# Kernel tuning notes

Measured on AMD Instinct MI355X. Metric: run time of the kernel, lower is better.

The kernel has to match this reference:

```python
import jax, jax.numpy as jnp
import numpy as np
from jax import lax

BETA_CONTENT = 1.0   # content_addressing default beta
BETA_TOPK = 10.0     # top_k_attention default beta
GAMMA = 1.5          # location sharpening
ERASE = 0.5          # erase_strength for write
EPS = 1e-8
NEG = -1.0e9

N_SLOTS, SLOT_D, BATCH, K = 65536, 256, 512, 64


def _l2norm(x):
    # F.normalize: x / max(||x||, 1e-12)
    n = jnp.sqrt(jnp.sum(x * x, axis=-1, keepdims=True))
    return x / jnp.maximum(n, 1e-12)


def setup_inputs() -> dict:
    key = jax.random.key(0)
    k1, k2, k3, k4, k5 = jax.random.split(key, 5)
    return {
        "memory": jax.random.normal(k1, (N_SLOTS, SLOT_D), dtype=jnp.float32) * 0.1,
        "query": jax.random.normal(k2, (BATCH, SLOT_D), dtype=jnp.float32),
        "value": jax.random.normal(k3, (BATCH, SLOT_D), dtype=jnp.float32),
        "prev_weights": jax.random.uniform(k4, (BATCH, N_SLOTS), dtype=jnp.float32),
        "shift_weights": jax.random.uniform(k5, (3,), dtype=jnp.float32),
        "k": K,
    }


def reference(memory, query, value, prev_weights, shift_weights, k):
    B, N = query.shape[0], memory.shape[0]
    # --- content addressing: cosine sim + softmax ---
    qn = _l2norm(query)                      # [B,D]
    mn = _l2norm(memory)                     # [N,D]
    sim = qn @ mn.T                          # [B,N]
    w_content = jax.nn.softmax(BETA_CONTENT * sim, axis=-1)
    read_content = w_content @ memory        # [B,D] read via content weights

    # --- top-k attention: soft threshold mask + softmax ---
    kk = min(int(k), N)
    topk_vals, _ = lax.top_k(sim, kk)        # [B,kk]
    thr = topk_vals[:, -1:]                  # kth largest similarity
    mask = jax.nn.sigmoid(BETA_TOPK * (sim - thr))
    w_topk = jax.nn.softmax(BETA_TOPK * sim + (1.0 - mask) * NEG, axis=-1)
    read_topk = w_topk @ memory              # [B,D]

    # --- location addressing: conv1d shift (padding=1) + gamma sharpen ---
    p = jnp.pad(prev_weights, ((0, 0), (1, 1)))  # [B,N+2]
    shifted = (p[:, :-2] * shift_weights[0]
               + p[:, 1:-1] * shift_weights[1]
               + p[:, 2:] * shift_weights[2])     # [B,N]
    sharp = shifted ** GAMMA
    w_loc = sharp / (jnp.sum(sharp, axis=-1, keepdims=True) + EPS)

    # --- write: softmax(address), multiplicative erase, additive write ---
    w_write = jax.nn.softmax(w_loc, axis=-1)          # write() softmaxes its input
    erase_factor = jnp.prod(1.0 - w_write * ERASE, axis=0)   # [N] sequential erases fused
    new_mem = memory * erase_factor[:, None] + w_write.T @ value  # [N,D]

    return jnp.concatenate([read_content.reshape(-1),
                            read_topk.reshape(-1),
                            new_mem.reshape(-1)])
```

## Files before the change

### kernel.cpp

```cpp
#include <hip/hip_runtime.h>
#include <math.h>

#define BATCH   512
#define NSLOTS  65536
#define DIM     256

#define RB      64
#define NROWG   (BATCH/RB)
#define NCG     64
#define CPG     (NSLOTS/NCG)
#define ST      32
#define NTILES  (CPG/ST)
#define DELTA   0.009f

#define WS_QN   0
#define WS_RN   (WS_QN + BATCH*DIM)
#define WS_WST  (WS_RN + NSLOTS)
#define WS_DEN  (WS_WST + BATCH*4)
#define WS_SST  (WS_DEN + BATCH)
#define WS_VT   (WS_SST + BATCH*NCG*16*4)
#define WS_MN   (WS_VT + (BATCH*DIM)/2)
#define WS_MT   (WS_MN + ((size_t)NSLOTS*DIM)/2)

typedef __attribute__((ext_vector_type(8))) short bf16x8;
typedef __attribute__((ext_vector_type(4))) float f32x4;

__device__ inline unsigned short f2b(float x){
  unsigned u = __float_as_uint(x);
  unsigned r = u + 0x7FFFu + ((u >> 16) & 1u);
  return (unsigned short)(r >> 16);
}
__device__ inline float b2f(unsigned short b){
  return __uint_as_float(((unsigned)b) << 16);
}

__device__ __forceinline__ void gl16(const void* g, void* l){
  __builtin_amdgcn_global_load_lds(
      (__attribute__((address_space(1))) void*)g,
      (__attribute__((address_space(3))) void*)l, 16, 0, 0);
}

#define SBAR_LGKM() do{ asm volatile("s_waitcnt lgkmcnt(0)" ::: "memory"); \
                        __builtin_amdgcn_s_barrier();                      \
                        asm volatile("" ::: "memory"); }while(0)
#define SBAR_ALL()  do{ asm volatile("s_waitcnt vmcnt(0) lgkmcnt(0)" ::: "memory"); \
                        __builtin_amdgcn_s_barrier();                               \
                        asm volatile("" ::: "memory"); }while(0)

__global__ __launch_bounds__(256) void k_qnorm(const float* __restrict__ q, float* __restrict__ qn){
  int b = blockIdx.x, t = threadIdx.x;
  float v = q[b*DIM + t];
  __shared__ float red[256];
  red[t] = v*v;
  __syncthreads();
  for (int s = 128; s > 0; s >>= 1){
    if (t < s) red[t] += red[t+s];
    __syncthreads();
  }
  float n = fmaxf(sqrtf(red[0]), 1e-12f);
  qn[b*DIM + t] = v / n;
}

__global__ __launch_bounds__(256) void k_mnprep(const float* __restrict__ mem,
                                                float* __restrict__ rn,
                                                unsigned short* __restrict__ MN){
  __shared__ float rns[64];
  int t = threadIdx.x;
  int s0 = blockIdx.x * 64;
  int w = t >> 6, ln = t & 63;
  #pragma unroll
  for (int it = 0; it < 16; ++it){
    int r = it*4 + w;
    float4 v = ((const float4*)(mem + (size_t)(s0 + r)*DIM))[ln];
    float s = v.x*v.x + v.y*v.y + v.z*v.z + v.w*v.w;
    #pragma unroll
    for (int off = 32; off > 0; off >>= 1) s += __shfl_xor(s, off, 64);
    if (ln == 0){
      float inv = 1.0f / fmaxf(sqrtf(s), 1e-12f);
      rns[r] = inv; rn[s0 + r] = inv;
    }
  }
  __syncthreads();
  #pragma unroll
  for (int j = 0; j < 8; ++j){
    int id = j*256 + t;
    int r = id >> 5;
    int c = id & 31;
    float inv = rns[r];
    const float4* p = (const float4*)(mem + (size_t)(s0 + r)*DIM + c*8);
    float4 a = p[0], b = p[1];
    bf16x8 o;
    o[0]=(short)f2b(a.x*inv); o[1]=(short)f2b(a.y*inv); o[2]=(short)f2b(a.z*inv); o[3]=(short)f2b(a.w*inv);
    o[4]=(short)f2b(b.x*inv); o[5]=(short)f2b(b.y*inv); o[6]=(short)f2b(b.z*inv); o[7]=(short)f2b(b.w*inv);
    *(bf16x8*)&MN[(size_t)(s0 + r)*DIM + ((c ^ (r & 7))*8)] = o;
  }
}

__global__ __launch_bounds__(256) void k_mtprep(const float* __restrict__ mem, unsigned short* __restrict__ MT){
  __shared__ __align__(16) unsigned short tile[64][68];
  int sb = (blockIdx.x >> 2)*64, dd = (blockIdx.x & 3)*64;
  int t = threadIdx.x;
  int w = t >> 6, ln = t & 63;
  #pragma unroll
  for (int k = 0; k < 4; ++k){
    int sl = w*16 + k*4 + (ln >> 4);
    int doff = (ln & 15)*4;
    float4 f = *(const float4*)&mem[(size_t)(sb + sl)*DIM + dd + doff];
    tile[doff+0][sl] = f2b(f.x);
    tile[doff+1][sl] = f2b(f.y);
    tile[doff+2][sl] = f2b(f.z);
    tile[doff+3][sl] = f2b(f.w);
  }
  __syncthreads();
  #pragma unroll
  for (int k = 0; k < 4; ++k){
    int dl = w*16 + k*4 + (ln >> 4);
    int boff = (ln & 15)*4;
    int B = boff >> 5;
    int p = (boff >> 3) & 3;
    int pp = p ^ ((dl >> 1) & 3);
    int off = B*32 + pp*8 + (boff & 7);
    *(short4*)&MT[(size_t)(dd + dl)*NSLOTS + sb + off] = *(const short4*)&tile[dl][boff];
  }
}

__global__ __launch_bounds__(256) void k_prep(const float* __restrict__ val, unsigned short* __restrict__ VT){
  __shared__ __align__(16) unsigned short tile[64][68];
  int bb = (blockIdx.x >> 2)*64, dd = (blockIdx.x & 3)*64;
  int t = threadIdx.x;
  int w = t >> 6, ln = t & 63;
  #pragma unroll
  for (int k = 0; k < 4; ++k){
    int bl = w*16 + k*4 + (ln >> 4);
    int doff = (ln & 15)*4;
    float4 f = *(const float4*)&val[(size_t)(bb + bl)*DIM + dd + doff];
    tile[doff+0][bl] = f2b(f.x);
    tile[doff+1][bl] = f2b(f.y);
    tile[doff+2][bl] = f2b(f.z);
    tile[doff+3][bl] = f2b(f.w);
  }
  __syncthreads();
  #pragma unroll
  for (int k = 0; k < 4; ++k){
    int dl = w*16 + k*4 + (ln >> 4);
    int boff = (ln & 15)*4;
    int c  = (bb + boff) >> 5;
    int p  = (boff >> 3) & 3;
    int pp = p ^ ((dl >> 1) & 3);
    size_t addr = (size_t)c*8192 + (size_t)(dd + dl)*32 + pp*8 + (boff & 7);
    *(short4*)&VT[addr] = *(const short4*)&tile[dl][boff];
  }
}

__global__ __launch_bounds__(256) void k_wstats(const float* __restrict__ prev, const float* __restrict__ sw,
                                                float* __restrict__ wst){
  int b = blockIdx.x, t = threadIdx.x;
  float s0 = sw[0], s1 = sw[1], s2 = sw[2];
  const float* p = prev + (size_t)b*NSLOTS;
  const float4* p4 = (const float4*)p;
  __shared__ float rs[256];
  float lsum = 0.f;
  for (int i4 = t; i4 < NSLOTS/4; i4 += 256){
    float4 f = p4[i4];
    float lft = (i4 > 0) ? p[4*i4 - 1] : 0.f;
    float rgt = (i4 < NSLOTS/4 - 1) ? p[4*i4 + 4] : 0.f;
    float sh0 = s0*lft + s1*f.x + s2*f.y;
    float sh1 = s0*f.x + s1*f.y + s2*f.z;
    float sh2 = s0*f.y + s1*f.z + s2*f.w;
    float sh3 = s0*f.z + s1*f.w + s2*rgt;
    lsum += sh0*sqrtf(sh0) + sh1*sqrtf(sh1) + sh2*sqrtf(sh2) + sh3*sqrtf(sh3);
  }
  rs[t] = lsum;
  __syncthreads();
  for (int s = 128; s > 0; s >>= 1){
    if (t < s) rs[t] += rs[t+s];
    __syncthreads();
  }
  float inv_d = 1.0f / (rs[0] + 1e-8f);
  __syncthreads();
  float lz = 0.f;
  for (int i4 = t; i4 < NSLOTS/4; i4 += 256){
    float4 f = p4[i4];
    float lft = (i4 > 0) ? p[4*i4 - 1] : 0.f;
    float rgt = (i4 < NSLOTS/4 - 1) ? p[4*i4 + 4] : 0.f;
    float sh0 = s0*lft + s1*f.x + s2*f.y;
    float sh1 = s0*f.x + s1*f.y + s2*f.z;
    float sh2 = s0*f.y + s1*f.z + s2*f.w;
    float sh3 = s0*f.z + s1*f.w + s2*rgt;
    lz += __expf(sh0*sqrtf(sh0)*inv_d) + __expf(sh1*sqrtf(sh1)*inv_d)
        + __expf(sh2*sqrtf(sh2)*inv_d) + __expf(sh3*sqrtf(sh3)*inv_d);
  }
  rs[t] = lz;
  __syncthreads();
  for (int s = 128; s > 0; s >>= 1){
    if (t < s) rs[t] += rs[t+s];
    __syncthreads();
  }
  if (t == 0){
    float4 o; o.x = inv_d; o.y = 1.0f/rs[0]; o.z = 0.f; o.w = 0.f;
    ((float4*)wst)[b] = o;
  }
}

__global__ __launch_bounds__(256) void k_wft(const float* __restrict__ prev, const float* __restrict__ sw,
                                             const float* __restrict__ wst, unsigned short* __restrict__ WFT){
  __shared__ __align__(16) unsigned short T[64][72];
  int bs = ((int)blockIdx.x & 7) * 64;
  int ss = ((int)blockIdx.x >> 3) * 64;
  int t = threadIdx.x;
  float s0 = sw[0], s1 = sw[1], s2 = sw[2];
  int rr = t >> 4;
  int cc = t & 15;
  #pragma unroll
  for (int pass = 0; pass < 4; ++pass){
    int bl = pass*16 + rr;
    int b = bs + bl;
    const float* p = prev + (size_t)b*NSLOTS + ss;
    float2 st = *(const float2*)&wst[b*4];
    int s = cc*4;
    float4 f = *(const float4*)(p + s);
    int gs = ss + s;
    float lft = (gs > 0) ? p[s-1] : 0.f;
    float rgt = (gs + 4 < NSLOTS) ? p[s+4] : 0.f;
    float sh0 = s0*lft + s1*f.x + s2*f.y;
    float sh1 = s0*f.x + s1*f.y + s2*f.z;
    float sh2 = s0*f.y + s1*f.z + s2*f.w;
    float sh3 = s0*f.z + s1*f.w + s2*rgt;
    T[s+0][bl] = f2b(__expf(sh0*sqrtf(sh0)*st.x)*st.y);
    T[s+1][bl] = f2b(__expf(sh1*sqrtf(sh1)*st.x)*st.y);
    T[s+2][bl] = f2b(__expf(sh2*sqrtf(sh2)*st.x)*st.y);
    T[s+3][bl] = f2b(__expf(sh3*sqrtf(sh3)*st.x)*st.y);
  }
  __syncthreads();
  int sr = t >> 3;
  int ch = t & 7;
  #pragma unroll
  for (int k = 0; k < 2; ++k){
    int row = k*32 + sr;
    int c  = (bs >> 5) + (ch >> 2);
    int pp = (ch & 3) ^ ((row >> 1) & 3);
    size_t addr = (size_t)(ss >> 6)*32768 + (size_t)c*2048 + (size_t)row*32 + pp*8;
    *(bf16x8*)&WFT[addr] = *(const bf16x8*)&T[row][ch*8];
  }
}

__global__ __launch_bounds__(256, 2) void k_simfused(
    const float* __restrict__ qn,
    const unsigned short* __restrict__ MN,
    const unsigned short* __restrict__ MT,
    float* __restrict__ outc, float* __restrict__ denom, float* __restrict__ sst)
{
  __shared__ __align__(16) unsigned short Ms[2][32*256];
  __shared__ __align__(16) unsigned short Md[2][256*32];
  __shared__ __align__(16) unsigned short Plds[64*40];

  int cg = blockIdx.x, rg = blockIdx.y;
  int t = threadIdx.x;
  int w = t >> 6;
  int lane = t & 63;
  int l = lane & 15;
  int q = lane >> 4;
  int row0 = rg * RB;

  bf16x8 qa[8];
  {
    int qrow = row0 + 16*w + l;
    #pragma unroll
    for (int kk = 0; kk < 8; ++kk){
      const float4* qp = (const float4*)&qn[(size_t)qrow*DIM + 32*kk + 8*q];
      float4 a0 = qp[0], a1 = qp[1];
      bf16x8 v;
      v[0]=(short)f2b(a0.x); v[1]=(short)f2b(a0.y); v[2]=(short)f2b(a0.z); v[3]=(short)f2b(a0.w);
      v[4]=(short)f2b(a1.x); v[5]=(short)f2b(a1.y); v[6]=(short)f2b(a1.z); v[7]=(short)f2b(a1.w);
      qa[kk] = v;
    }
  }

  const char* msP = (const char*)MN + (size_t)cg*CPG*512 + (size_t)w*4096 + (size_t)lane*16;
  const char* mtP = (const char*)MT + (size_t)(w*64 + (lane>>2))*((size_t)NSLOTS*2)
                                    + (size_t)cg*CPG*2 + (size_t)(lane&3)*16;

  auto STAGE = [&](int tl, int buf){
    size_t mso = (size_t)tl*16384;
    size_t mto = (size_t)tl*64;
    #pragma unroll
    for (int j = 0; j < 4; ++j)
      gl16(msP + mso + (size_t)j*1024, &Ms[buf][w*2048 + j*512]);
    #pragma unroll
    for (int j = 0; j < 4; ++j)
      gl16(mtP + mto + (size_t)j*2097152, &Md[buf][w*2048 + j*512]);
  };

  f32x4 accO[16];
  #pragma unroll
  for (int c = 0; c < 16; ++c) accO[c] = (f32x4){0.f,0.f,0.f,0.f};

  float dsum[4] = {0.f,0.f,0.f,0.f};
  float tv0[4] = {-1e30f,-1e30f,-1e30f,-1e30f}, tv1[4] = {-1e30f,-1e30f,-1e30f,-1e30f};
  int   ti0[4] = {0,0,0,0}, ti1[4] = {0,0,0,0};

  STAGE(0, 0);
  SBAR_ALL();

  int r7 = l & 7;
  int sw2 = (q ^ ((l >> 1) & 3)) * 8;

  for (int tile = 0; tile < NTILES; ++tile){
    int cur = tile & 1;
    if (tile + 1 < NTILES) STAGE(tile + 1, cur ^ 1);
    int i0 = cg*CPG + tile*ST;

    const unsigned short* msb = &Ms[cur][0];
    f32x4 S0 = (f32x4){0.f,0.f,0.f,0.f}, S1 = (f32x4){0.f,0.f,0.f,0.f};
    #pragma unroll
    for (int kk = 0; kk < 8; ++kk){
      int c0 = ((4*kk + q) ^ r7) * 8;
      bf16x8 b0 = *(const bf16x8*)&msb[(l     )*256 + c0];
      bf16x8 b1 = *(const bf16x8*)&msb[(16 + l)*256 + c0];
      S0 = __builtin_amdgcn_mfma_f32_16x16x32_bf16(qa[kk], b0, S0, 0, 0, 0);
      S1 = __builtin_amdgcn_mfma_f32_16x16x32_bf16(qa[kk], b1, S1, 0, 0, 0);
    }

    #pragma unroll
    for (int c = 0; c < 2; ++c){
      int slot = i0 + 16*c + l;
      #pragma unroll
      for (int reg = 0; reg < 4; ++reg){
        float v = (c == 0) ? S0[reg] : S1[reg];
        bool g0 = v > tv0[reg];
        bool g1 = v > tv1[reg];
        float ov0 = tv0[reg]; int oi0 = ti0[reg];
        tv1[reg] = g0 ? ov0 : (g1 ? v : tv1[reg]);
        ti1[reg] = g0 ? oi0 : (g1 ? slot : ti1[reg]);
        tv0[reg] = g0 ? v : tv0[reg];
        ti0[reg] = g0 ? slot : ti0[reg];
        unsigned short wb = f2b(__expf(v));
        dsum[reg] += b2f(wb);
        Plds[(16*w + 4*q + reg)*40 + 16*c + l] = (short)wb;
      }
    }
    SBAR_LGKM();

    bf16x8 pa = *(const bf16x8*)&Plds[(16*w + l)*40 + 8*q];
    const unsigned short* mdb = &Md[cur][0];
    #pragma unroll
    for (int ct = 0; ct < 16; ++ct){
      bf16x8 b = *(const bf16x8*)&mdb[(16*ct + l)*32 + sw2];
      accO[ct] = __builtin_amdgcn_mfma_f32_16x16x32_bf16(pa, b, accO[ct], 0, 0, 0);
    }
    SBAR_ALL();
  }

  #pragma unroll
  for (int reg = 0; reg < 4; ++reg){
    float s = dsum[reg];
    s += __shfl_xor(s, 1, 64); s += __shfl_xor(s, 2, 64);
    s += __shfl_xor(s, 4, 64); s += __shfl_xor(s, 8, 64);
    if (l == 0) atomicAdd(&denom[row0 + 16*w + 4*q + reg], s);
  }
  #pragma unroll
  for (int reg = 0; reg < 4; ++reg){
    int row = row0 + 16*w + 4*q + reg;
    size_t base = (((size_t)row*NCG + cg)*16 + l)*2;
    float2* S2 = (float2*)sst;
    S2[base + 0] = make_float2(tv0[reg], __int_as_float(ti0[reg]));
    S2[base + 1] = make_float2(tv1[reg], __int_as_float(ti1[reg]));
  }
  #pragma unroll
  for (int ct = 0; ct < 16; ++ct){
    #pragma unroll
    for (int reg = 0; reg < 4; ++reg){
      int row = row0 + 16*w + 4*q + reg;
      atomicAdd(&outc[(size_t)row*DIM + 16*ct + l], accO[ct][reg]);
    }
  }
}

__global__ __launch_bounds__(256) void k_finish(const float* __restrict__ sst, const float* __restrict__ denom,
                                                const float* __restrict__ qn, const float* __restrict__ rn,
                                                const float* __restrict__ mem,
                                                float* __restrict__ outc, float* __restrict__ outk){
  int row = blockIdx.x, t = threadIdx.x;
  __shared__ float red[256];
  __shared__ int cnt;
  __shared__ int cidx[128];
  __shared__ float csim[128];
  __shared__ int bestIdx;
  const float2* S = (const float2*)sst + (size_t)row*NCG*16*2;
  float2 e[8];
  float lmax = -1e30f;
  #pragma unroll
  for (int k = 0; k < 8; ++k){ e[k] = S[t*8 + k]; lmax = fmaxf(lmax, e[k].x); }
  red[t] = lmax;
  __syncthreads();
  for (int s = 128; s > 0; s >>= 1){
    if (t < s) red[t] = fmaxf(red[t], red[t+s]);
    __syncthreads();
  }
  float M = red[0];
  if (t == 0) cnt = 0;
  __syncthreads();
  #pragma unroll
  for (int k = 0; k < 8; ++k){
    if (e[k].x >= M - DELTA){
      int p = atomicAdd(&cnt, 1);
      if (p < 128) cidx[p] = __float_as_int(e[k].y);
    }
  }
  __syncthreads();
  int n = min(cnt, 128);
  int wv = t >> 6, ln = t & 63;
  for (int ci = wv; ci < n; ci += 4){
    int slot = cidx[ci];
    float4 a = ((const float4*)&qn[(size_t)row*DIM])[ln];
    float4 b = ((const float4*)&mem[(size_t)slot*DIM])[ln];
    float s = a.x*b.x + a.y*b.y + a.z*b.z + a.w*b.w;
    #pragma unroll
    for (int off = 32; off > 0; off >>= 1) s += __shfl_xor(s, off, 64);
    if (ln == 0) csim[ci] = s * rn[slot];
  }
  __syncthreads();
  if (t == 0){
    float bv = -1e30f; int bi = 0x7fffffff;
    for (int i = 0; i < n; ++i){
      float v = csim[i]; int id = cidx[i];
      if (v > bv || (v == bv && id < bi)){ bv = v; bi = id; }
    }
    bestIdx = bi;
  }
  __syncthreads();
  float inv = 1.0f / denom[row];
  outc[(size_t)row*DIM + t] *= inv;
  outk[(size_t)row*DIM + t] = mem[(size_t)bestIdx*DIM + t];
}

__global__ __launch_bounds__(256, 4) void k_newmem(const float* __restrict__ mem,
                                                const unsigned short* __restrict__ VT2,
                                                const unsigned short* __restrict__ WFT2,
                                                float* __restrict__ outm){
  __shared__ __align__(16) unsigned short VB[2][256*32];
  __shared__ __align__(16) unsigned short WB[2][64*32];

  int t = threadIdx.x;
  int i0 = blockIdx.x * 64;
  int w = t >> 6;
  int lane = t & 63;
  int l = lane & 15, q = lane >> 4;

  const char* vbase = (const char*)VT2 + (size_t)w*4096 + (size_t)lane*16;
  const char* wbase = (const char*)WFT2 + (size_t)blockIdx.x*65536 + (size_t)w*1024 + (size_t)lane*16;

  auto STAGE = [&](int c, int buf){
    #pragma unroll
    for (int j = 0; j < 4; ++j)
      gl16(vbase + (size_t)c*16384 + (size_t)j*1024, &VB[buf][w*2048 + j*512]);
    gl16(wbase + (size_t)c*4096, &WB[buf][w*512]);
  };

  f32x4 accO[16];
  #pragma unroll
  for (int c = 0; c < 16; ++c) accO[c] = (f32x4){0.f,0.f,0.f,0.f};
  float epl = 1.0f;

  STAGE(0, 0);
  SBAR_ALL();

  int sw2 = (q ^ ((l >> 1) & 3)) * 8;

  #pragma unroll 1
  for (int c = 0; c < 16; ++c){
    int cur = c & 1;
    if (c + 1 < 16) STAGE(c + 1, cur ^ 1);
    bf16x8 af = *(const bf16x8*)&WB[cur][(16*w + l)*32 + sw2];
    #pragma unroll
    for (int j = 0; j < 8; ++j)
      epl *= (1.0f - 0.5f*b2f((unsigned short)af[j]));
    #pragma unroll
    for (int ct = 0; ct < 16; ++ct){
      bf16x8 bfg = *(const bf16x8*)&VB[cur][(16*ct + l)*32 + sw2];
      accO[ct] = __builtin_amdgcn_mfma_f32_16x16x32_bf16(af, bfg, accO[ct], 0, 0, 0);
    }
    SBAR_ALL();
  }

  epl *= __shfl_xor(epl, 16, 64);
  epl *= __shfl_xor(epl, 32, 64);

  #pragma unroll
  for (int reg = 0; reg < 4; ++reg){
    int so = i0 + 16*w + 4*q + reg;
    float e = __shfl(epl, 4*q + reg, 64);
    #pragma unroll
    for (int ct = 0; ct < 16; ++ct){
      int d = 16*ct + l;
      outm[(size_t)so*DIM + d] = mem[(size_t)so*DIM + d]*e + accO[ct][reg];
    }
  }
}

extern "C" void kernel_launch(void* const* d_in, const int* in_sizes, int n_in,
                              void* d_out, int out_size, void* d_ws, size_t ws_size,
                              hipStream_t stream){
  const float* mem  = (const float*)d_in[0];
  const float* qry  = (const float*)d_in[1];
  const float* val  = (const float*)d_in[2];
  const float* prev = (const float*)d_in[3];
  const float* sw   = (const float*)d_in[4];
  float* out = (float*)d_out;
  float* ws  = (float*)d_ws;

  float* qn   = ws + WS_QN;
  float* rn   = ws + WS_RN;
  float* wst  = ws + WS_WST;
  float* den  = ws + WS_DEN;
  float* sst  = ws + WS_SST;
  unsigned short* VT = (unsigned short*)(ws + WS_VT);
  unsigned short* MN = (unsigned short*)(ws + WS_MN);
  unsigned short* MT = (unsigned short*)(ws + WS_MT);
  unsigned short* WFT = MN;

  float* out_content = out;
  float* out_topk    = out + BATCH*DIM;
  float* out_newmem  = out + 2*BATCH*DIM;

  hipMemsetAsync(out_content, 0, BATCH*DIM*sizeof(float), stream);
  hipMemsetAsync(den, 0, BATCH*sizeof(float), stream);
  hipLaunchKernelGGL(k_qnorm,   dim3(BATCH),       dim3(DIM), 0, stream, qry, qn);
  hipLaunchKernelGGL(k_mnprep,  dim3(NSLOTS/64),   dim3(256), 0, stream, mem, rn, MN);
  hipLaunchKernelGGL(k_mtprep,  dim3((NSLOTS/64)*4), dim3(256), 0, stream, mem, MT);
  hipLaunchKernelGGL(k_prep,    dim3(32),          dim3(256), 0, stream, val, VT);
  hipLaunchKernelGGL(k_wstats,  dim3(BATCH),       dim3(256), 0, stream, prev, sw, wst);
  hipLaunchKernelGGL(k_simfused,dim3(NCG, NROWG),  dim3(256), 0, stream, qn, MN, MT, out_content, den, sst);
  hipLaunchKernelGGL(k_wft,     dim3((NSLOTS/64)*(BATCH/64)), dim3(256), 0, stream, prev, sw, wst, WFT);
  hipLaunchKernelGGL(k_finish,  dim3(BATCH),       dim3(256), 0, stream, sst, den, qn, rn, mem, out_content, out_topk);
  hipLaunchKernelGGL(k_newmem,  dim3(NSLOTS/64),   dim3(256), 0, stream, mem, VT, WFT, out_newmem);
}
```

Before: 522.6 us.

## Split per-row weight statistics into chunked kernels with atomic reductions

Replaces the single k_wstats kernel, which ran one 256-thread block per batch row, with two kernels. Each processes 16 chunks per row (8192 blocks) and combines partial sums through wave shuffles and atomicAdd, followed by a small kernel that finalizes the inverse normalizers. The aim is to expose more parallelism over the 128 MB prev_weights stream so the bandwidth-bound statistics pass fills the GPU better than 512 blocks could. In exchange it adds two launches, a memset, and float atomics whose summation order is nondeterministic.

```diff
diff --git a/kernel.cpp b/kernel.cpp
--- a/kernel.cpp
+++ b/kernel.cpp
@@ -17,7 +17,9 @@
 #define WS_RN   (WS_QN + BATCH*DIM)
 #define WS_WST  (WS_RN + NSLOTS)
 #define WS_DEN  (WS_WST + BATCH*4)
-#define WS_SST  (WS_DEN + BATCH)
+#define WS_ZS   (WS_DEN + BATCH)
+#define WS_ZZ   (WS_ZS + BATCH)
+#define WS_SST  (WS_ZZ + BATCH)
 #define WS_VT   (WS_SST + BATCH*NCG*16*4)
 #define WS_MN   (WS_VT + (BATCH*DIM)/2)
 #define WS_MT   (WS_MN + ((size_t)NSLOTS*DIM)/2)
@@ -152,15 +154,19 @@
   }
 }
 
-__global__ __launch_bounds__(256) void k_wstats(const float* __restrict__ prev, const float* __restrict__ sw,
-                                                float* __restrict__ wst){
-  int b = blockIdx.x, t = threadIdx.x;
+__global__ __launch_bounds__(256) void k_ws1(const float* __restrict__ prev, const float* __restrict__ sw,
+                                             float* __restrict__ zs){
+  int blk = blockIdx.x;
+  int b = blk >> 4, ch = blk & 15;
+  int t = threadIdx.x;
+  int w = t >> 6, lane = t & 63;
   float s0 = sw[0], s1 = sw[1], s2 = sw[2];
   const float* p = prev + (size_t)b*NSLOTS;
   const float4* p4 = (const float4*)p;
-  __shared__ float rs[256];
   float lsum = 0.f;
-  for (int i4 = t; i4 < NSLOTS/4; i4 += 256){
+  #pragma unroll
+  for (int k = 0; k < 4; ++k){
+    int i4 = ch*1024 + k*256 + t;
     float4 f = p4[i4];
     float lft = (i4 > 0) ? p[4*i4 - 1] : 0.f;
     float rgt = (i4 < NSLOTS/4 - 1) ? p[4*i4 + 4] : 0.f;
@@ -170,16 +176,28 @@
     float sh3 = s0*f.z + s1*f.w + s2*rgt;
     lsum += sh0*sqrtf(sh0) + sh1*sqrtf(sh1) + sh2*sqrtf(sh2) + sh3*sqrtf(sh3);
   }
-  rs[t] = lsum;
-  __syncthreads();
-  for (int s = 128; s > 0; s >>= 1){
-    if (t < s) rs[t] += rs[t+s];
-    __syncthreads();
-  }
-  float inv_d = 1.0f / (rs[0] + 1e-8f);
-  __syncthreads();
+  #pragma unroll
+  for (int off = 32; off > 0; off >>= 1) lsum += __shfl_xor(lsum, off, 64);
+  __shared__ float wsum[4];
+  if (lane == 0) wsum[w] = lsum;
+  __syncthreads();
+  if (t == 0) atomicAdd(&zs[b], wsum[0] + wsum[1] + wsum[2] + wsum[3]);
+}
+
+__global__ __launch_bounds__(256) void k_ws2(const float* __restrict__ prev, const float* __restrict__ sw,
+                                             const float* __restrict__ zs, float* __restrict__ zz){
+  int blk = blockIdx.x;
+  int b = blk >> 4, ch = blk & 15;
+  int t = threadIdx.x;
+  int w = t >> 6, lane = t & 63;
+  float s0 = sw[0], s1 = sw[1], s2 = sw[2];
+  float inv_d = 1.0f / (zs[b] + 1e-8f);
+  const float* p = prev + (size_t)b*NSLOTS;
+  const float4* p4 = (const float4*)p;
   float lz = 0.f;
-  for (int i4 = t; i4 < NSLOTS/4; i4 += 256){
+  #pragma unroll
+  for (int k = 0; k < 4; ++k){
+    int i4 = ch*1024 + k*256 + t;
     float4 f = p4[i4];
     float lft = (i4 > 0) ? p[4*i4 - 1] : 0.f;
     float rgt = (i4 < NSLOTS/4 - 1) ? p[4*i4 + 4] : 0.f;
@@ -190,16 +208,22 @@
     lz += __expf(sh0*sqrtf(sh0)*inv_d) + __expf(sh1*sqrtf(sh1)*inv_d)
         + __expf(sh2*sqrtf(sh2)*inv_d) + __expf(sh3*sqrtf(sh3)*inv_d);
   }
-  rs[t] = lz;
-  __syncthreads();
-  for (int s = 128; s > 0; s >>= 1){
-    if (t < s) rs[t] += rs[t+s];
-    __syncthreads();
-  }
-  if (t == 0){
-    float4 o; o.x = inv_d; o.y = 1.0f/rs[0]; o.z = 0.f; o.w = 0.f;
-    ((float4*)wst)[b] = o;
-  }
+  #pragma unroll
+  for (int off = 32; off > 0; off >>= 1) lz += __shfl_xor(lz, off, 64);
+  __shared__ float wsum[4];
+  if (lane == 0) wsum[w] = lz;
+  __syncthreads();
+  if (t == 0) atomicAdd(&zz[b], wsum[0] + wsum[1] + wsum[2] + wsum[3]);
+}
+
+__global__ __launch_bounds__(256) void k_invd(const float* __restrict__ zs, const float* __restrict__ zz,
+                                              float* __restrict__ wst){
+  int b = blockIdx.x*256 + threadIdx.x;
+  float4 o;
+  o.x = 1.0f / (zs[b] + 1e-8f);
+  o.y = 1.0f / zz[b];
+  o.z = 0.f; o.w = 0.f;
+  ((float4*)wst)[b] = o;
 }
 
 __global__ __launch_bounds__(256) void k_wft(const float* __restrict__ prev, const float* __restrict__ sw,
@@ -513,6 +537,8 @@
   float* rn   = ws + WS_RN;
   float* wst  = ws + WS_WST;
   float* den  = ws + WS_DEN;
+  float* zs   = ws + WS_ZS;
+  float* zz   = ws + WS_ZZ;
   float* sst  = ws + WS_SST;
   unsigned short* VT = (unsigned short*)(ws + WS_VT);
   unsigned short* MN = (unsigned short*)(ws + WS_MN);
@@ -525,11 +551,14 @@
 
   hipMemsetAsync(out_content, 0, BATCH*DIM*sizeof(float), stream);
   hipMemsetAsync(den, 0, BATCH*sizeof(float), stream);
+  hipMemsetAsync(zs, 0, 2*BATCH*sizeof(float), stream);
   hipLaunchKernelGGL(k_qnorm,   dim3(BATCH),       dim3(DIM), 0, stream, qry, qn);
   hipLaunchKernelGGL(k_mnprep,  dim3(NSLOTS/64),   dim3(256), 0, stream, mem, rn, MN);
   hipLaunchKernelGGL(k_mtprep,  dim3((NSLOTS/64)*4), dim3(256), 0, stream, mem, MT);
   hipLaunchKernelGGL(k_prep,    dim3(32),          dim3(256), 0, stream, val, VT);
-  hipLaunchKernelGGL(k_wstats,  dim3(BATCH),       dim3(256), 0, stream, prev, sw, wst);
+  hipLaunchKernelGGL(k_ws1,     dim3(BATCH*16),    dim3(256), 0, stream, prev, sw, zs);
+  hipLaunchKernelGGL(k_ws2,     dim3(BATCH*16),    dim3(256), 0, stream, prev, sw, zs, zz);
+  hipLaunchKernelGGL(k_invd,    dim3(BATCH/256),   dim3(256), 0, stream, zs, zz, wst);
   hipLaunchKernelGGL(k_simfused,dim3(NCG, NROWG),  dim3(256), 0, stream, qn, MN, MT, out_content, den, sst);
   hipLaunchKernelGGL(k_wft,     dim3((NSLOTS/64)*(BATCH/64)), dim3(256), 0, stream, prev, sw, wst, WFT);
   hipLaunchKernelGGL(k_finish,  dim3(BATCH),       dim3(256), 0, stream, sst, den, qn, rn, mem, out_content, out_topk);
```

Measured after the change: 495.1 us. -5.3%, faster.
